# Optimization experiments

Measured on AMD Instinct MI355X. Metric: run time of the kernel, lower is better.

The kernel has to match this reference:

```python
import jax, jax.numpy as jnp
import numpy as np

N, D = 8192, 1024
MAX_REP = 8

def setup_inputs() -> dict:
    key = jax.random.key(0)
    k1, k2 = jax.random.split(key)
    encoder_h = jax.random.normal(k1, (N, D), dtype=jnp.float32)
    repeats = jax.random.randint(k2, (N,), 0, MAX_REP, dtype=jnp.int32)
    return {"encoder_h": encoder_h, "repeats": repeats}

def reference(encoder_h, repeats):
    # Variable-length repeat_interleave along axis 0.
    # Equivalent to tf tile+sequence_mask+boolean_mask+reshape in the original,
    # but expressed as a single cumsum-index gather (no max_repeat-sized blowup).
    repeats = repeats.astype(jnp.int32)
    total = int(jnp.sum(repeats))  # dynamic output length (data-dependent)
    csum = jnp.cumsum(repeats)                     # [N]
    # row index for each output slot: searchsorted maps output position -> source row
    idx = jnp.searchsorted(csum, jnp.arange(total, dtype=jnp.int32), side='right')  # [total]
    return encoder_h[idx]                          # [total, D]
```

## Files before the change

kernel.cpp:

```cpp
#include <hip/hip_runtime.h>


typedef float nfloat4 __attribute__((ext_vector_type(4)));

#define SCAN_THREADS 1024
#define ELEMS_PER_THREAD 8

__global__ __launch_bounds__(SCAN_THREADS)
void scan_kernel(const int* __restrict__ repeats,
                 int* __restrict__ csum_excl, int n) {
    __shared__ int wsum[SCAN_THREADS / 64];
    const int t = threadIdx.x;
    const int lane = t & 63;
    const int wave = t >> 6;
    const int base = t * ELEMS_PER_THREAD;

    int vals[ELEMS_PER_THREAD];
    int s = 0;
#pragma unroll
    for (int j = 0; j < ELEMS_PER_THREAD; ++j) {
        const int idx = base + j;
        const int v = (idx < n) ? repeats[idx] : 0;
        vals[j] = v;
        s += v;
    }
    int isum = s;
#pragma unroll
    for (int off = 1; off < 64; off <<= 1) {
        const int v = __shfl_up(isum, off, 64);
        if (lane >= off) isum += v;
    }
    if (lane == 63) wsum[wave] = isum;
    __syncthreads();
    if (t == 0) {
        int acc = 0;
#pragma unroll
        for (int w = 0; w < SCAN_THREADS / 64; ++w) {
            const int v = wsum[w];
            wsum[w] = acc;
            acc += v;
        }
    }
    __syncthreads();
    int run = wsum[wave] + isum - s;
#pragma unroll
    for (int j = 0; j < ELEMS_PER_THREAD; ++j) {
        const int idx = base + j;
        if (idx < n) csum_excl[idx] = run;
        run += vals[j];
    }
}

__global__ __launch_bounds__(256)
void spread_rows_kernel(const nfloat4* __restrict__ h,
                        const int* __restrict__ repeats,
                        const int* __restrict__ csum_excl,
                        nfloat4* __restrict__ out,
                        int d4 ) {
    const int row = blockIdx.x;
    const int r = repeats[row];
    if (r == 0) return;
    const int obase = csum_excl[row];
    const nfloat4* __restrict__ src = h + (size_t)row * d4;
    nfloat4* __restrict__ dst0 = out + (size_t)obase * d4;
    for (int i = threadIdx.x; i < d4; i += blockDim.x) {
        const nfloat4 v = src[i];
        for (int k = 0; k < r; ++k) {
            dst0[(size_t)k * d4 + i] = v;
        }
    }
}

extern "C" void kernel_launch(void* const* d_in, const int* in_sizes, int n_in,
                              void* d_out, int out_size, void* d_ws, size_t ws_size,
                              hipStream_t stream) {
    const float* encoder_h = (const float*)d_in[0];
    const int*   repeats   = (const int*)d_in[1];
    float*       out       = (float*)d_out;

    const int n = in_sizes[1];
    const int d = in_sizes[0] / n;

    int* csum_excl = (int*)d_ws;

    scan_kernel<<<1, SCAN_THREADS, 0, stream>>>(repeats, csum_excl, n);
    spread_rows_kernel<<<n, 256, 0, stream>>>(
        (const nfloat4*)encoder_h, repeats, csum_excl, (nfloat4*)out, d / 4);
}
```

Before: 155.3 us.

## Fuse prefix scan into spread kernel with per-block redundant reduction

Removes the separate single-block scan kernel. Each block instead recomputes its output offset by summing all earlier repeats with vectorized loads and a wave/block reduction. Each block now handles four rows, loading all four source vectors before issuing the repeated stores. This drops one launch and the serial single-block scan. In exchange, every block performs redundant prefix-sum work that grows with its position, which is quadratic in total but small next to the data copy. The bulk path assumes rbase is a multiple of four, which holds because CHUNK is 4.

```diff
diff --git a/kernel.cpp b/kernel.cpp
--- a/kernel.cpp
+++ b/kernel.cpp
@@ -3,70 +3,64 @@
 
 typedef float nfloat4 __attribute__((ext_vector_type(4)));
 
-#define SCAN_THREADS 1024
-#define ELEMS_PER_THREAD 8
+#define CHUNK 4
+#define BLOCK 256
 
-__global__ __launch_bounds__(SCAN_THREADS)
-void scan_kernel(const int* __restrict__ repeats,
-                 int* __restrict__ csum_excl, int n) {
-    __shared__ int wsum[SCAN_THREADS / 64];
+__global__ __launch_bounds__(BLOCK)
+void spread_fused_kernel(const nfloat4* __restrict__ h,
+                         const int* __restrict__ repeats,
+                         nfloat4* __restrict__ out,
+                         int n, int d4 ) {
+    const int rbase = blockIdx.x * CHUNK;
     const int t = threadIdx.x;
     const int lane = t & 63;
     const int wave = t >> 6;
-    const int base = t * ELEMS_PER_THREAD;
 
-    int vals[ELEMS_PER_THREAD];
-    int s = 0;
-#pragma unroll
-    for (int j = 0; j < ELEMS_PER_THREAD; ++j) {
-        const int idx = base + j;
-        const int v = (idx < n) ? repeats[idx] : 0;
-        vals[j] = v;
-        s += v;
-    }
-    int isum = s;
-#pragma unroll
-    for (int off = 1; off < 64; off <<= 1) {
-        const int v = __shfl_up(isum, off, 64);
-        if (lane >= off) isum += v;
-    }
-    if (lane == 63) wsum[wave] = isum;
-    __syncthreads();
-    if (t == 0) {
-        int acc = 0;
-#pragma unroll
-        for (int w = 0; w < SCAN_THREADS / 64; ++w) {
-            const int v = wsum[w];
-            wsum[w] = acc;
-            acc += v;
+    __shared__ int wpart[BLOCK / 64];
+    int local = 0;
+    {
+        const int nq = rbase >> 2;
+        const int4* rp4 = (const int4*)repeats;
+        for (int q = t; q < nq; q += BLOCK) {
+            const int4 v = rp4[q];
+            local += v.x + v.y + v.z + v.w;
         }
     }
+#pragma unroll
+    for (int off = 32; off > 0; off >>= 1)
+        local += __shfl_down(local, off, 64);
+    if (lane == 0) wpart[wave] = local;
     __syncthreads();
-    int run = wsum[wave] + isum - s;
+    const int obase = wpart[0] + wpart[1] + wpart[2] + wpart[3];
+
+    int reps[CHUNK];
+    if (rbase + CHUNK <= n) {
+        const int4 r4 = *(const int4*)(repeats + rbase);
+        reps[0] = r4.x; reps[1] = r4.y; reps[2] = r4.z; reps[3] = r4.w;
+    } else {
 #pragma unroll
-    for (int j = 0; j < ELEMS_PER_THREAD; ++j) {
-        const int idx = base + j;
-        if (idx < n) csum_excl[idx] = run;
-        run += vals[j];
+        for (int j = 0; j < CHUNK; ++j)
+            reps[j] = (rbase + j < n) ? repeats[rbase + j] : 0;
     }
-}
+    int offs[CHUNK];
+    offs[0] = obase;
+#pragma unroll
+    for (int j = 1; j < CHUNK; ++j) offs[j] = offs[j - 1] + reps[j - 1];
 
-__global__ __launch_bounds__(256)
-void spread_rows_kernel(const nfloat4* __restrict__ h,
-                        const int* __restrict__ repeats,
-                        const int* __restrict__ csum_excl,
-                        nfloat4* __restrict__ out,
-                        int d4 ) {
-    const int row = blockIdx.x;
-    const int r = repeats[row];
-    if (r == 0) return;
-    const int obase = csum_excl[row];
-    const nfloat4* __restrict__ src = h + (size_t)row * d4;
-    nfloat4* __restrict__ dst0 = out + (size_t)obase * d4;
-    for (int i = threadIdx.x; i < d4; i += blockDim.x) {
-        const nfloat4 v = src[i];
-        for (int k = 0; k < r; ++k) {
-            dst0[(size_t)k * d4 + i] = v;
+    for (int i = t; i < d4; i += BLOCK) {
+        nfloat4 v[CHUNK];
+#pragma unroll
+        for (int j = 0; j < CHUNK; ++j) {
+            const int row = rbase + j;
+            v[j] = (row < n) ? h[(size_t)row * d4 + i] : nfloat4{0, 0, 0, 0};
+        }
+#pragma unroll
+        for (int j = 0; j < CHUNK; ++j) {
+            const int r = reps[j];
+            nfloat4* __restrict__ dst = out + (size_t)offs[j] * d4 + i;
+            for (int k = 0; k < r; ++k) {
+                dst[(size_t)k * d4] = v[j];
+            }
         }
     }
 }
@@ -81,9 +75,7 @@
     const int n = in_sizes[1];
     const int d = in_sizes[0] / n;
 
-    int* csum_excl = (int*)d_ws;
-
-    scan_kernel<<<1, SCAN_THREADS, 0, stream>>>(repeats, csum_excl, n);
-    spread_rows_kernel<<<n, 256, 0, stream>>>(
-        (const nfloat4*)encoder_h, repeats, csum_excl, (nfloat4*)out, d / 4);
+    const int nblocks = (n + CHUNK - 1) / CHUNK;
+    spread_fused_kernel<<<nblocks, BLOCK, 0, stream>>>(
+        (const nfloat4*)encoder_h, repeats, (nfloat4*)out, n, d / 4);
 }
```

After: 144.1 us. 7.2% less time.
